# Kernel optimization log

Hardware: AMD Instinct MI355X
Metric: run time of the kernel (lower is better)

The kernel has to match this reference:

```python
import jax, jax.numpy as jnp
import numpy as np
import math

D = 1024
B, S = 8, 2048


def setup_inputs() -> dict:
    key = jax.random.key(0)
    ks = jax.random.split(key, 8)
    q = jax.random.normal(ks[0], (B, S, D), dtype=jnp.float32)
    k = jax.random.normal(ks[1], (B, S, D), dtype=jnp.float32)
    v1 = jax.random.normal(ks[2], (B, S, D), dtype=jnp.float32)
    mask = jax.random.normal(ks[3], (1, S, S), dtype=jnp.float32)
    # Linear params: torch Linear stores W as [out, in]; init ~ U(-1/sqrt(in), 1/sqrt(in))
    lim = 1.0 / math.sqrt(D)
    W1 = jax.random.uniform(ks[4], (D, D), jnp.float32, -lim, lim)
    b1 = jax.random.uniform(ks[5], (D,), jnp.float32, -lim, lim)
    W2 = jax.random.uniform(ks[6], (D, D), jnp.float32, -lim, lim)
    b2 = jax.random.uniform(ks[7], (D,), jnp.float32, -lim, lim)
    return {"q": q, "k": k, "v1": v1, "mask": mask,
            "W1": W1, "b1": b1, "W2": W2, "b2": b2}


def _proj(x, W1, b1, W2, b2):
    # linear2(linear1(x)); torch Linear: x @ W.T + b
    h = jnp.einsum('bsd,od->bso', x, W1) + b1
    return jnp.einsum('bsd,od->bso', h, W2) + b2


def reference(q, k, v1, mask, W1, b1, W2, b2):
    qp = _proj(q, W1, b1, W2, b2)          # [B,S,D]
    kp = _proj(k, W1, b1, W2, b2)          # [B,S,D]
    scale = 1.0 / math.sqrt(qp.shape[-1])
    qk = jnp.einsum('bqd,bkd->bqk', qp, kp) * scale  # [B,S,S]
    qk = qk + mask                          # broadcast [1,S,S]
    attn = jax.nn.softmax(qk, axis=-1)
    return jnp.einsum('bqk,bkd->bqd', attn, v1)  # [B,S,D]
```

## Files before the change

kernel.cpp:

```cpp
#include <hip/hip_runtime.h>
#include <hip/hip_bf16.h>

typedef __hip_bfloat16 bf16;
typedef short short8 __attribute__((ext_vector_type(8)));
typedef float f32x4 __attribute__((ext_vector_type(4)));

constexpr int Bn = 8, Sn = 2048, Dn = 1024;
constexpr int BM = 256, BN = 256, BK = 64;

__global__ void cast_f32_bf16_k(const float* __restrict__ x, bf16* __restrict__ y, int n) {
  int i = (blockIdx.x * blockDim.x + threadIdx.x) * 4;
  if (i >= n) return;
  float4 f = *reinterpret_cast<const float4*>(x + i);
  bf16 tmp[4] = {__float2bfloat16(f.x), __float2bfloat16(f.y),
                 __float2bfloat16(f.z), __float2bfloat16(f.w)};
  *reinterpret_cast<short4*>(y + i) = *reinterpret_cast<const short4*>(tmp);
}

__global__ void transpose_cast_v_k(const float* __restrict__ v, bf16* __restrict__ vt) {
  __shared__ float tile[32][33];
  const int s0 = blockIdx.x * 32, d0 = blockIdx.y * 32, b = blockIdx.z;
  const float* src = v + (size_t)b * Sn * Dn;
  bf16* dst = vt + (size_t)b * Dn * Sn;
  const int tx = threadIdx.x & 31, ty = threadIdx.x >> 5;
  #pragma unroll
  for (int i = 0; i < 4; ++i) {
    int s = ty + i * 8;
    tile[s][tx] = src[(size_t)(s0 + s) * Dn + d0 + tx];
  }
  __syncthreads();
  #pragma unroll
  for (int i = 0; i < 4; ++i) {
    int d = ty + i * 8;
    dst[(size_t)(d0 + d) * Sn + s0 + tx] = __float2bfloat16(tile[tx][d]);
  }
}

#define BARRIER() asm volatile("s_barrier" ::: "memory")

#define QUAD(ms, ns) do {                                                     \
    __builtin_amdgcn_s_setprio(1);                                            \
    _Pragma("unroll")                                                         \
    for (int mi4 = 0; mi4 < 4; ++mi4) {                                       \
      _Pragma("unroll")                                                       \
      for (int n2 = 0; n2 < 2; ++n2) {                                        \
        _Pragma("unroll")                                                     \
        for (int kk = 0; kk < 2; ++kk)                                        \
          asm volatile("v_mfma_f32_16x16x32_bf16 %0, %1, %2, %0"              \
                       : "+v"(acc[(ms)*4+mi4][(ns)*2+n2])                     \
                       : "v"(aF[mi4][kk]), "v"(bF[(ns)*2+n2][kk]));           \
      }                                                                       \
    }                                                                         \
    __builtin_amdgcn_s_setprio(0);                                            \
  } while (0)

#define RD_A(buf, ms) do {                                                    \
    _Pragma("unroll")                                                         \
    for (int mi4 = 0; mi4 < 4; ++mi4) {                                       \
      aF[mi4][0] = rdA(buf, ms, mi4, 0);                                      \
      aF[mi4][1] = rdA(buf, ms, mi4, 1);                                      \
    }                                                                         \
  } while (0)

#define RD_B(buf, ns) do {                                                    \
    bF[(ns)*2  ][0] = rdB(buf, ns, 0, 0);                                     \
    bF[(ns)*2  ][1] = rdB(buf, ns, 0, 1);                                     \
    bF[(ns)*2+1][0] = rdB(buf, ns, 1, 0);                                     \
    bF[(ns)*2+1][1] = rdB(buf, ns, 1, 1);                                     \
  } while (0)

template<int EPI>
__global__ __launch_bounds__(512, 2)
void gemm256_k(const bf16* __restrict__ A, const bf16* __restrict__ BT,
               void* __restrict__ Cv, const float* __restrict__ aux,
               int N, int K, long long sAz, long long sBz, long long sCz,
               float scale, int gx, int gy)
{
  __shared__ __align__(128) bf16 sh[4 * 16384];

  const int nwg = (int)gridDim.x;
  const int flat = (int)blockIdx.x;
  const int swz = (flat & 7) * (nwg >> 3) + (flat >> 3);
  const int tn = swz % gx;
  const int rem = swz / gx;
  const int tm = rem % gy;
  const int z  = rem / gy;

  const int t = threadIdx.x, w = t >> 6, lane = t & 63;
  const int wm = w >> 2, wn = w & 3;
  const int fr = lane & 15, kg = lane >> 4;
  const int m0 = tm * BM, n0 = tn * BN;
  const bf16* Abase = A + (size_t)z * sAz + (size_t)m0 * K;
  const bf16* Bbase = BT + (size_t)z * sBz + (size_t)n0 * K;

  f32x4 acc[8][4];
  const f32x4 fz = {0.f, 0.f, 0.f, 0.f};
  #pragma unroll
  for (int i = 0; i < 8; ++i)
    #pragma unroll
    for (int j = 0; j < 4; ++j) acc[i][j] = fz;
  short8 aF[4][2], bF[4][2];

  auto stage = [&](int dstElemBase, const bf16* gbase, int half, int kt) {
    const bf16* g0 = gbase + (size_t)(half * 128) * K + (size_t)kt * BK;
    bf16* db = (bf16*)sh + dstElemBase + half * 8192;
    #pragma unroll
    for (int i = 0; i < 2; ++i) {
      const int s0 = i * 512 + w * 64;
      const int slot = s0 + lane;
      const int row = slot >> 3;
      const int cb = (slot & 7) ^ (row & 7);
      const bf16* src = g0 + (size_t)row * K + cb * 8;
      __builtin_amdgcn_global_load_lds((__attribute__((address_space(1))) void*)src,
          (__attribute__((address_space(3))) void*)(db + s0 * 8), 16, 0, 0);
    }
  };
  auto rdA = [&](int buf, int ms, int mi4, int kk) -> short8 {
    const int row = wm * 128 + ms * 64 + mi4 * 16 + fr;
    int loc = row * 128 + kk * 64 + kg * 16;
    loc ^= (row & 7) << 4;
    return *reinterpret_cast<const short8*>((const char*)sh + buf * 32768 + loc);
  };
  auto rdB = [&](int buf, int ns, int j, int kk) -> short8 {
    const int row = wn * 64 + ns * 32 + j * 16 + fr;
    int loc = row * 128 + kk * 64 + kg * 16;
    loc ^= (row & 7) << 4;
    return *reinterpret_cast<const short8*>((const char*)sh + 65536 + buf * 32768 + loc);
  };

  const int NT = K / BK;
  stage(32768, Bbase, 0, 0); stage(32768, Bbase, 1, 0);
  stage(0,     Abase, 0, 0); stage(0,     Abase, 1, 0);
  stage(49152, Bbase, 0, 1); stage(49152, Bbase, 1, 1);
  asm volatile("s_waitcnt vmcnt(4)" ::: "memory");
  BARRIER();

  int T = 0;
  for (; T < NT - 2; T += 2) {
    RD_A(0, 0); RD_B(0, 0);
    stage(16384, Abase, 0, T + 1);
    BARRIER(); QUAD(0, 0); BARRIER();

    RD_B(0, 1);
    stage(16384, Abase, 1, T + 1);
    BARRIER(); QUAD(0, 1); BARRIER();

    RD_A(0, 1);
    stage(32768, Bbase, 0, T + 2);
    BARRIER(); QUAD(1, 0); BARRIER();

    stage(32768, Bbase, 1, T + 2);
    asm volatile("s_waitcnt vmcnt(4)" ::: "memory");
    BARRIER(); QUAD(1, 1); BARRIER();

    RD_A(1, 0); RD_B(1, 0);
    stage(0, Abase, 0, T + 2);
    BARRIER(); QUAD(0, 0); BARRIER();

    RD_B(1, 1);
    stage(0, Abase, 1, T + 2);
    BARRIER(); QUAD(0, 1); BARRIER();

    RD_A(1, 1);
    stage(49152, Bbase, 0, T + 3);
    BARRIER(); QUAD(1, 0); BARRIER();

    stage(49152, Bbase, 1, T + 3);
    asm volatile("s_waitcnt vmcnt(4)" ::: "memory");
    BARRIER(); QUAD(1, 1); BARRIER();
  }
  {
    RD_A(0, 0); RD_B(0, 0);
    stage(16384, Abase, 0, T + 1);
    BARRIER(); QUAD(0, 0); BARRIER();

    RD_B(0, 1);
    stage(16384, Abase, 1, T + 1);
    BARRIER(); QUAD(0, 1); BARRIER();

    RD_A(0, 1);
    BARRIER(); QUAD(1, 0); BARRIER();

    asm volatile("s_waitcnt vmcnt(0)" ::: "memory");
    BARRIER(); QUAD(1, 1); BARRIER();

    RD_A(1, 0); RD_B(1, 0);
    BARRIER(); QUAD(0, 0); BARRIER();

    RD_B(1, 1);
    BARRIER(); QUAD(0, 1); BARRIER();

    RD_A(1, 1);
    BARRIER(); QUAD(1, 0); BARRIER();

    BARRIER(); QUAD(1, 1); BARRIER();
  }

  const int or0 = kg * 4;
  if constexpr (EPI == 0) {
    bf16* C = (bf16*)Cv + (size_t)z * sCz;
    #pragma unroll
    for (int mi = 0; mi < 8; ++mi)
      #pragma unroll
      for (int r = 0; r < 4; ++r) {
        const int row = m0 + wm * 128 + mi * 16 + or0 + r;
        #pragma unroll
        for (int ni = 0; ni < 4; ++ni) {
          const int col = n0 + wn * 64 + ni * 16 + fr;
          C[(size_t)row * N + col] = __float2bfloat16(acc[mi][ni][r] + aux[col]);
        }
      }
  } else if constexpr (EPI == 1) {
    bf16* C = (bf16*)Cv + (size_t)z * sCz;
    #pragma unroll
    for (int mi = 0; mi < 8; ++mi)
      #pragma unroll
      for (int r = 0; r < 4; ++r) {
        const int row = m0 + wm * 128 + mi * 16 + or0 + r;
        #pragma unroll
        for (int ni = 0; ni < 4; ++ni) {
          const int col = n0 + wn * 64 + ni * 16 + fr;
          float v = acc[mi][ni][r] * scale + aux[(size_t)row * N + col];
          C[(size_t)row * N + col] = __float2bfloat16(v);
        }
      }
  } else {
    float* C = (float*)Cv + (size_t)z * sCz;
    #pragma unroll
    for (int mi = 0; mi < 8; ++mi)
      #pragma unroll
      for (int r = 0; r < 4; ++r) {
        const int row = m0 + wm * 128 + mi * 16 + or0 + r;
        #pragma unroll
        for (int ni = 0; ni < 4; ++ni) {
          const int col = n0 + wn * 64 + ni * 16 + fr;
          C[(size_t)row * N + col] = acc[mi][ni][r];
        }
      }
  }
}

__global__ __launch_bounds__(256)
void softmax_rows_k(bf16* __restrict__ sc) {
  const size_t row = blockIdx.x;
  bf16* p = sc + row * (size_t)Sn;
  const int t = threadIdx.x;
  unsigned short raw[8];
  *reinterpret_cast<int4*>(raw) = *reinterpret_cast<const int4*>(p + t * 8);
  float x[8];
  float m = -1e30f;
  #pragma unroll
  for (int j = 0; j < 8; ++j) {
    x[j] = __uint_as_float(((unsigned)raw[j]) << 16);
    m = fmaxf(m, x[j]);
  }
  #pragma unroll
  for (int off = 32; off >= 1; off >>= 1) m = fmaxf(m, __shfl_xor(m, off));
  __shared__ float sred[4], ssum[4];
  const int w = t >> 6;
  if ((t & 63) == 0) sred[w] = m;
  __syncthreads();
  m = fmaxf(fmaxf(sred[0], sred[1]), fmaxf(sred[2], sred[3]));
  float e[8], s = 0.f;
  #pragma unroll
  for (int j = 0; j < 8; ++j) { e[j] = __expf(x[j] - m); s += e[j]; }
  #pragma unroll
  for (int off = 32; off >= 1; off >>= 1) s += __shfl_xor(s, off);
  if ((t & 63) == 0) ssum[w] = s;
  __syncthreads();
  s = (ssum[0] + ssum[1]) + (ssum[2] + ssum[3]);
  const float inv = 1.f / s;
  unsigned short o[8];
  #pragma unroll
  for (int j = 0; j < 8; ++j) {
    bf16 hv = __float2bfloat16(e[j] * inv);
    o[j] = *reinterpret_cast<unsigned short*>(&hv);
  }
  *reinterpret_cast<int4*>(p + t * 8) = *reinterpret_cast<const int4*>(o);
}

extern "C" void kernel_launch(void* const* d_in, const int* in_sizes, int n_in,
                              void* d_out, int out_size, void* d_ws, size_t ws_size,
                              hipStream_t stream) {
  const float* q    = (const float*)d_in[0];
  const float* k    = (const float*)d_in[1];
  const float* v1   = (const float*)d_in[2];
  const float* mask = (const float*)d_in[3];
  const float* W1   = (const float*)d_in[4];
  const float* b1   = (const float*)d_in[5];
  const float* W2   = (const float*)d_in[6];
  const float* b2   = (const float*)d_in[7];
  float* out = (float*)d_out;

  const size_t nQKD = (size_t)Bn * Sn * Dn;
  char* ws = (char*)d_ws;
  bf16* qkb = (bf16*)ws;
  bf16* qb  = qkb;
  bf16* kb  = qkb + nQKD;
  bf16* vtb = qkb + 2 * nQKD;
  bf16* hb  = vtb + nQKD;
  bf16* w1b = hb + 2 * nQKD;
  bf16* w2b = w1b + (size_t)Dn * Dn;
  bf16* scb = w2b + (size_t)Dn * Dn;

  dim3 blk(256);
  const int nQK = (int)nQKD;
  cast_f32_bf16_k<<<dim3(nQK / 4 / 256), blk, 0, stream>>>(q, qb, nQK);
  cast_f32_bf16_k<<<dim3(nQK / 4 / 256), blk, 0, stream>>>(k, kb, nQK);
  cast_f32_bf16_k<<<dim3(Dn * Dn / 4 / 256), blk, 0, stream>>>(W1, w1b, Dn * Dn);
  cast_f32_bf16_k<<<dim3(Dn * Dn / 4 / 256), blk, 0, stream>>>(W2, w2b, Dn * Dn);
  transpose_cast_v_k<<<dim3(Sn / 32, Dn / 32, Bn), blk, 0, stream>>>(v1, vtb);

  const int M2 = 2 * Bn * Sn;
  dim3 gblk(512);
  gemm256_k<0><<<dim3(4 * (M2 / BM)), gblk, 0, stream>>>(
      qkb, w1b, hb, b1, Dn, Dn, 0, 0, 0, 1.f, 4, M2 / BM);
  gemm256_k<0><<<dim3(4 * (M2 / BM)), gblk, 0, stream>>>(
      hb, w2b, qkb, b2, Dn, Dn, 0, 0, 0, 1.f, 4, M2 / BM);
  gemm256_k<1><<<dim3(8 * 8 * Bn), gblk, 0, stream>>>(
      qb, kb, scb, mask, Sn, Dn,
      (long long)Sn * Dn, (long long)Sn * Dn, (long long)Sn * Sn, 0.03125f, 8, 8);
  softmax_rows_k<<<dim3(Bn * Sn), blk, 0, stream>>>(scb);
  gemm256_k<2><<<dim3(4 * 8 * Bn), gblk, 0, stream>>>(
      scb, vtb, out, nullptr, Dn, Sn,
      (long long)Sn * Sn, (long long)Dn * Sn, (long long)Sn * Dn, 1.f, 4, 8);
}
```

Measured before the change: 387.5 us.

## Restructure GEMM main loop to prefetch a full tile ahead with deeper vmcnt

Rewrites the GEMM K-loop so both A and B for the next tile are loaded in the prologue, and each tile body issues all global stages for tile T+2 after the last reads from the current buffer. The wait depth moves from vmcnt(4) to vmcnt(8), keeping more global loads in flight and decoupling A/B loads from the current tile's LDS reads. The MFMA loop order is also changed to iterate kk outermost. The schedule becomes simpler, but stage placement is delayed until late in each tile, which could expose latency if the prefetch distance proves insufficient.

```diff
diff --git a/kernel.cpp b/kernel.cpp
--- a/kernel.cpp
+++ b/kernel.cpp
@@ -37,15 +37,17 @@
 }
 
 #define BARRIER() asm volatile("s_barrier" ::: "memory")
+#define WAIT_VM8() asm volatile("s_waitcnt vmcnt(8)" ::: "memory")
+#define WAIT_VM0() asm volatile("s_waitcnt vmcnt(0)" ::: "memory")
 
 #define QUAD(ms, ns) do {                                                     \
     __builtin_amdgcn_s_setprio(1);                                            \
     _Pragma("unroll")                                                         \
-    for (int mi4 = 0; mi4 < 4; ++mi4) {                                       \
+    for (int kk = 0; kk < 2; ++kk) {                                          \
       _Pragma("unroll")                                                       \
-      for (int n2 = 0; n2 < 2; ++n2) {                                        \
+      for (int mi4 = 0; mi4 < 4; ++mi4) {                                     \
         _Pragma("unroll")                                                     \
-        for (int kk = 0; kk < 2; ++kk)                                        \
+        for (int n2 = 0; n2 < 2; ++n2)                                        \
           asm volatile("v_mfma_f32_16x16x32_bf16 %0, %1, %2, %0"              \
                        : "+v"(acc[(ms)*4+mi4][(ns)*2+n2])                     \
                        : "v"(aF[mi4][kk]), "v"(bF[(ns)*2+n2][kk]));           \
@@ -67,6 +69,22 @@
     bF[(ns)*2  ][1] = rdB(buf, ns, 0, 1);                                     \
     bF[(ns)*2+1][0] = rdB(buf, ns, 1, 0);                                     \
     bF[(ns)*2+1][1] = rdB(buf, ns, 1, 1);                                     \
+  } while (0)
+
+#define TILE_BODY(cc, DS, Tn2, WAITCODE) do {                                 \
+    RD_A(cc, 0); RD_B(cc, 0);                                                 \
+    BARRIER(); QUAD(0, 0); BARRIER();                                         \
+    RD_B(cc, 1);                                                              \
+    BARRIER(); QUAD(0, 1); BARRIER();                                         \
+    RD_A(cc, 1);                                                              \
+    if (DS) stage(32768 + (cc)*16384, Bbase, 0, (Tn2));                       \
+    BARRIER(); QUAD(1, 0); BARRIER();                                         \
+    if (DS) { stage(32768 + (cc)*16384, Bbase, 1, (Tn2));                     \
+              stage((cc)*16384,          Abase, 0, (Tn2));                    \
+              stage((cc)*16384,          Abase, 1, (Tn2)); }                  \
+    BARRIER(); QUAD(1, 1);                                                    \
+    WAITCODE;                                                                 \
+    BARRIER();                                                                \
   } while (0)
 
 template<int EPI>
@@ -132,69 +150,17 @@
   stage(32768, Bbase, 0, 0); stage(32768, Bbase, 1, 0);
   stage(0,     Abase, 0, 0); stage(0,     Abase, 1, 0);
   stage(49152, Bbase, 0, 1); stage(49152, Bbase, 1, 1);
-  asm volatile("s_waitcnt vmcnt(4)" ::: "memory");
+  stage(16384, Abase, 0, 1); stage(16384, Abase, 1, 1);
+  WAIT_VM8();
   BARRIER();
 
   int T = 0;
   for (; T < NT - 2; T += 2) {
-    RD_A(0, 0); RD_B(0, 0);
-    stage(16384, Abase, 0, T + 1);
-    BARRIER(); QUAD(0, 0); BARRIER();
-
-    RD_B(0, 1);
-    stage(16384, Abase, 1, T + 1);
-    BARRIER(); QUAD(0, 1); BARRIER();
-
-    RD_A(0, 1);
-    stage(32768, Bbase, 0, T + 2);
-    BARRIER(); QUAD(1, 0); BARRIER();
-
-    stage(32768, Bbase, 1, T + 2);
-    asm volatile("s_waitcnt vmcnt(4)" ::: "memory");
-    BARRIER(); QUAD(1, 1); BARRIER();
-
-    RD_A(1, 0); RD_B(1, 0);
-    stage(0, Abase, 0, T + 2);
-    BARRIER(); QUAD(0, 0); BARRIER();
-
-    RD_B(1, 1);
-    stage(0, Abase, 1, T + 2);
-    BARRIER(); QUAD(0, 1); BARRIER();
-
-    RD_A(1, 1);
-    stage(49152, Bbase, 0, T + 3);
-    BARRIER(); QUAD(1, 0); BARRIER();
-
-    stage(49152, Bbase, 1, T + 3);
-    asm volatile("s_waitcnt vmcnt(4)" ::: "memory");
-    BARRIER(); QUAD(1, 1); BARRIER();
-  }
-  {
-    RD_A(0, 0); RD_B(0, 0);
-    stage(16384, Abase, 0, T + 1);
-    BARRIER(); QUAD(0, 0); BARRIER();
-
-    RD_B(0, 1);
-    stage(16384, Abase, 1, T + 1);
-    BARRIER(); QUAD(0, 1); BARRIER();
-
-    RD_A(0, 1);
-    BARRIER(); QUAD(1, 0); BARRIER();
-
-    asm volatile("s_waitcnt vmcnt(0)" ::: "memory");
-    BARRIER(); QUAD(1, 1); BARRIER();
-
-    RD_A(1, 0); RD_B(1, 0);
-    BARRIER(); QUAD(0, 0); BARRIER();
-
-    RD_B(1, 1);
-    BARRIER(); QUAD(0, 1); BARRIER();
-
-    RD_A(1, 1);
-    BARRIER(); QUAD(1, 0); BARRIER();
-
-    BARRIER(); QUAD(1, 1); BARRIER();
-  }
+    TILE_BODY(0, (T     < NT - 2), T + 2, WAIT_VM8());
+    TILE_BODY(1, (T + 1 < NT - 2), T + 3, WAIT_VM8());
+  }
+  TILE_BODY(0, 0, 0, WAIT_VM0());
+  TILE_BODY(1, 0, 0, (void)0);
 
   const int or0 = kg * 4;
   if constexpr (EPI == 0) {
```

New measurement: 398.3 us. +2.8%, slower.
